# Kernel optimization log

Measured on AMD Instinct MI355X. Metric: run time of the kernel, lower is better.

Reference implementation:

```python
import jax, jax.numpy as jnp
import numpy as np

N_SIGMA = 2
FG_W = 1.0
W_INST, W_VAR, W_SEED = 1.0, 10.0, 1.0
N_IDS = 15  # instance ids 1..15 (0 = background)


def _xym(H, W, dtype):
    # torch buffer: xm varies along width, ym along height, linspace over 512 then sliced
    xm = jnp.broadcast_to(jnp.linspace(0.0, 1.0, 512)[:W][None, :], (H, W))
    ym = jnp.broadcast_to(jnp.linspace(0.0, 1.0, 512)[:H][:, None], (H, W))
    return jnp.stack([xm, ym], 0).astype(dtype)  # [2,H,W]


def _lovasz_hinge_flat(logits, gt):
    # canonical Lovasz hinge over a flat image; gt in {0,1} float
    signs = 2.0 * gt - 1.0
    errors = 1.0 - logits * signs
    order = jnp.argsort(-errors)
    errors_sorted = errors[order]
    gt_sorted = gt[order]
    gts = gt_sorted.sum()
    inter = gts - jnp.cumsum(gt_sorted)
    union = gts + jnp.cumsum(1.0 - gt_sorted)
    jacc = 1.0 - inter / union
    grad = jnp.concatenate([jacc[:1], jacc[1:] - jacc[:-1]])
    return jnp.dot(jax.nn.relu(errors_sorted), jax.lax.stop_gradient(grad))


def _loss(prediction, instances, labels):
    B, C, H, W = prediction.shape
    xym = _xym(H, W, prediction.dtype)
    spatial_emb = jnp.tanh(prediction[:, 0:2]) + xym           # [B,2,H,W]
    sigma = prediction[:, 2:2 + N_SIGMA]                       # [B,2,H,W]
    seed = jax.nn.sigmoid(prediction[:, 2 + N_SIGMA])          # [B,H,W]

    ids = jnp.arange(1, N_IDS + 1)
    maskf = (instances[:, None] == ids[None, :, None, None]).astype(prediction.dtype)  # [B,N,H,W]
    counts = maskf.sum((-2, -1))                               # [B,N]
    valid = counts > 0
    safe = jnp.maximum(counts, 1.0)

    centers = jnp.einsum('bchw,bnhw->bnc', spatial_emb, maskf) / safe[..., None]  # [B,N,2]
    s_mean = jnp.einsum('bchw,bnhw->bnc', sigma, maskf) / safe[..., None]         # [B,N,2]
    s_sg = jax.lax.stop_gradient(s_mean)

    # sum over mask of (sigma - s_sg)^2, expanded to avoid a [B,N,2,H,W] tensor
    e2 = jnp.einsum('bchw,bnhw->bnc', sigma * sigma, maskf)
    var_sum = e2 - 2.0 * s_sg * (s_mean * safe[..., None]) + s_sg * s_sg * counts[..., None]
    var_i = var_sum.sum(-1) / (N_SIGMA * safe)                 # torch.mean over [n_sigma, M]

    s_exp = jnp.exp(10.0 * s_mean)                             # [B,N,2] (grad flows, as in torch)
    dist_arg = jnp.zeros((B, N_IDS, H, W), prediction.dtype)
    for c in range(N_SIGMA):  # tiny fixed loop over 2 coordinate channels
        d = spatial_emb[:, c][:, None] - centers[:, :, c][..., None, None]
        dist_arg = dist_arg + s_exp[:, :, c][..., None, None] * d * d
    dist = jnp.exp(-dist_arg)                                  # [B,N,H,W]

    logits = (dist * 2.0 - 1.0).reshape(B * N_IDS, H * W)
    labs = maskf.reshape(B * N_IDS, H * W)
    inst_i = jax.vmap(_lovasz_hinge_flat)(logits, labs).reshape(B, N_IDS)

    seed_i = FG_W * jnp.einsum('bnhw,bnhw->bn', maskf,
                               (seed[:, None] - jax.lax.stop_gradient(dist)) ** 2)

    bg = (labels == 0).astype(prediction.dtype)
    seed_bg = jnp.einsum('bhw,bhw->b', bg, seed * seed)        # (seed - 0)^2 on background

    vf = valid.astype(prediction.dtype)
    obj = jnp.maximum(vf.sum(1), 1.0)
    inst_b = (vf * inst_i).sum(1) / obj
    var_b = (vf * var_i).sum(1) / obj
    seed_b = (seed_bg + (vf * seed_i).sum(1)) / (H * W)
    return jnp.mean(W_INST * inst_b + W_VAR * var_b + W_SEED * seed_b)


def setup_inputs() -> dict:
    key = jax.random.key(0)
    k1, k2, k3 = jax.random.split(key, 3)
    prediction = jax.random.normal(k1, (16, 5, 512, 512), dtype=jnp.float32)
    instances = jax.random.randint(k2, (16, 512, 512), 0, 16, dtype=jnp.int64)
    labels = jax.random.randint(k3, (16, 512, 512), 0, 2, dtype=jnp.int64)
    return {"prediction": prediction, "instances": instances, "labels": labels}


def reference(prediction, instances, labels):
    return _loss(prediction, instances, labels)
```

## Files before the change

### kernel.cpp

```cpp
#include <hip/hip_runtime.h>
#include <hip/hip_fp16.h>
#include <cmath>

#define BATCH 16
#define NID   15
#define NSEG  240
#define HW    262144
#define HEADB 65536
#define NSPL  8
#define NCHK  4
#define PREBLK 512
#define PSTRIDE 112

#define KFINEBASE 30208
#define KOVF 119
#define KTOT 2424

__device__ __forceinline__ int keyof(float d) {
  unsigned b = __float_as_uint(d);
  return (b >= 0x3B800000u) ? (int)((b >> 15) - KFINEBASE + KOVF) : (int)(b >> 23);
}
__device__ __forceinline__ void boundsof(int k, float* lo, float* hi) {
  if (k >= KOVF) {
    unsigned u = (unsigned)(k - KOVF + KFINEBASE) << 15;
    *lo = __uint_as_float(u);
    *hi = __uint_as_float(u + 32768u);
  } else {
    *lo = __uint_as_float((unsigned)k << 23);
    *hi = __uint_as_float((unsigned)(k + 1) << 23);
  }
}

__device__ __forceinline__ float fast_tanh(float x) {
  float e = __expf(2.0f * x);
  return 1.0f - 2.0f / (e + 1.0f);
}
__device__ __forceinline__ float fast_sigmoid(float x) {
  return 1.0f / (1.0f + __expf(-x));
}

struct Params { float cx, cy, e0, e1, var, valid, cnt; };
__device__ __forceinline__ Params calc_params(const float* __restrict__ st) {
  Params p;
  float cnt = st[0];
  float safe = fmaxf(cnt, 1.0f);
  p.cx = st[1] / safe;
  p.cy = st[2] / safe;
  float m0 = st[3] / safe, m1 = st[4] / safe;
  float v0 = st[5] - 2.0f * m0 * (m0 * safe) + m0 * m0 * cnt;
  float v1 = st[6] - 2.0f * m1 * (m1 * safe) + m1 * m1 * cnt;
  p.var = (v0 + v1) / (2.0f * safe);
  p.e0 = expf(10.0f * m0);
  p.e1 = expf(10.0f * m1);
  p.valid = (cnt > 0.f) ? 1.f : 0.f;
  p.cnt = cnt;
  return p;
}

__global__ void __launch_bounds__(256, 2)
pre_kernel(const float* __restrict__ pred, const int* __restrict__ inst,
           const int* __restrict__ lab, float* __restrict__ blockpart,
           unsigned* __restrict__ exyh, unsigned* __restrict__ tb8,
           unsigned* __restrict__ sd8) {
  __shared__ float ws[4][NID * 7 + 1];
  int tid = threadIdx.x;
  int w = tid >> 6, lane = tid & 63;
  int gid = blockIdx.x;
  int b = gid >> 5, c = gid & 31;
  const float* pb = pred + (size_t)b * 5 * HW;
  const int4* ip = (const int4*)(inst + (size_t)b * HW);
  const int4* lp = (const int4*)(lab + (size_t)b * HW);
  size_t bq = (size_t)b * (HW / 4);
  float acc[NID][7];
#pragma unroll
  for (int id = 0; id < NID; ++id)
#pragma unroll
    for (int s = 0; s < 7; ++s) acc[id][s] = 0.f;
  float bgacc = 0.f;
  for (int it = 0; it < 8; ++it) {
    int g = c * 2048 + it * 256 + tid;
    float4 v0 = ((const float4*)pb)[g];
    float4 v1 = ((const float4*)(pb + HW))[g];
    float4 v2 = ((const float4*)(pb + 2 * HW))[g];
    float4 v3 = ((const float4*)(pb + 3 * HW))[g];
    float4 v4 = ((const float4*)(pb + 4 * HW))[g];
    int4 t4 = ip[g];
    int4 l4 = lp[g];
    float p0a[4] = {v0.x, v0.y, v0.z, v0.w};
    float p1a[4] = {v1.x, v1.y, v1.z, v1.w};
    float p2a[4] = {v2.x, v2.y, v2.z, v2.w};
    float p3a[4] = {v3.x, v3.y, v3.z, v3.w};
    float p4a[4] = {v4.x, v4.y, v4.z, v4.w};
    int ta[4] = {t4.x, t4.y, t4.z, t4.w};
    int la[4] = {l4.x, l4.y, l4.z, l4.w};
    unsigned eo[4], tpack = 0, spack = 0;
    int px0 = g * 4;
#pragma unroll
    for (int k = 0; k < 4; ++k) {
      int px = px0 + k;
      float xm = (float)(px & 511) * (1.0f / 511.0f);
      float ym = (float)(px >> 9) * (1.0f / 511.0f);
      float ex = fast_tanh(p0a[k]) + xm;
      float ey = fast_tanh(p1a[k]) + ym;
      float sd = fast_sigmoid(p4a[k]);
      __half2 h = __floats2half2_rn(ex, ey);
      eo[k] = *reinterpret_cast<unsigned*>(&h);
      int t = ta[k];
      tpack |= ((unsigned)(t & 255)) << (8 * k);
      unsigned sq = (unsigned)(sd * 255.0f + 0.5f);
      spack |= (sq & 255u) << (8 * k);
      float p2 = p2a[k], p3 = p3a[k];
      float q2 = p2 * p2, q3 = p3 * p3;
#pragma unroll
      for (int id = 0; id < NID; ++id) {
        float pr = (t == id + 1) ? 1.0f : 0.0f;
        acc[id][0] += pr;
        acc[id][1] += pr * ex;
        acc[id][2] += pr * ey;
        acc[id][3] += pr * p2;
        acc[id][4] += pr * p3;
        acc[id][5] += pr * q2;
        acc[id][6] += pr * q3;
      }
      if (la[k] == 0) bgacc += sd * sd;
    }
    ((uint4*)exyh)[bq + g] = make_uint4(eo[0], eo[1], eo[2], eo[3]);
    tb8[bq + g] = tpack;
    sd8[bq + g] = spack;
  }
#pragma unroll
  for (int id = 0; id < NID; ++id)
#pragma unroll
    for (int s = 0; s < 7; ++s) {
      float v = acc[id][s];
      for (int off = 32; off > 0; off >>= 1) v += __shfl_down(v, off, 64);
      if (lane == 0) ws[w][id * 7 + s] = v;
    }
  for (int off = 32; off > 0; off >>= 1) bgacc += __shfl_down(bgacc, off, 64);
  if (lane == 0) ws[w][NID * 7] = bgacc;
  __syncthreads();
  float* bp = blockpart + (size_t)gid * PSTRIDE;
  for (int i = tid; i < NID * 7 + 1; i += 256)
    bp[i] = ws[0][i] + ws[1][i] + ws[2][i] + ws[3][i];
}

__global__ void reduce_kernel(const float* __restrict__ blockpart, float* __restrict__ stats,
                              float* __restrict__ seedbg) {
  int s = blockIdx.x;
  int b = blockIdx.y;
  int tid = threadIdx.x;
  float v = (tid < 32) ? blockpart[(size_t)(b * 32 + tid) * PSTRIDE + s] : 0.f;
  for (int off = 32; off > 0; off >>= 1) v += __shfl_down(v, off, 64);
  if (tid == 0) {
    if (s < NID * 7) {
      int id = s / 7, st = s % 7;
      stats[(b * NID + id) * 8 + st] = v;
    } else {
      seedbg[b] = v;
    }
  }
}

__global__ void __launch_bounds__(512)
hist_kernel(const unsigned* __restrict__ exyh, const unsigned* __restrict__ tb8,
            const unsigned* __restrict__ sd8, const float* __restrict__ stats,
            unsigned* __restrict__ partPN, float* __restrict__ seedi) {
  int split = blockIdx.x;
  int chunk = blockIdx.y;
  int b = blockIdx.z;
  int seg0 = chunk * 4;
  __shared__ unsigned lhist[4 * KTOT];
  __shared__ float prm[4][5];
  int tid = threadIdx.x;
  if (tid < 4) {
    int gs = seg0 + tid;
    if (gs < NID) {
      Params pp = calc_params(stats + (size_t)(b * NID + gs) * 8);
      prm[tid][0] = pp.cx; prm[tid][1] = pp.cy; prm[tid][2] = pp.e0; prm[tid][3] = pp.e1;
      prm[tid][4] = pp.valid;
    } else {
      prm[tid][4] = 0.f;
    }
  }
  for (int k = tid; k < 4 * KTOT; k += 512) lhist[k] = 0u;
  __syncthreads();
  float cxr[4], cyr[4], e0r[4], e1r[4];
  bool vr[4];
#pragma unroll
  for (int n = 0; n < 4; ++n) {
    cxr[n] = prm[n][0]; cyr[n] = prm[n][1]; e0r[n] = prm[n][2]; e1r[n] = prm[n][3];
    vr[n] = (prm[n][4] != 0.f);
  }
  const uint4* ev = (const uint4*)exyh + (size_t)b * (HW / 4);
  const unsigned* tv = tb8 + (size_t)b * (HW / 4);
  const unsigned* sv = sd8 + (size_t)b * (HW / 4);
  int lane = tid & 63;
  int wid = tid >> 6;
  int swl = (lane * 21) & 63;
  float sacc[4] = {0.f, 0.f, 0.f, 0.f};
  int g = split * 8192 + wid * 64 + swl;
  uint4 ee = ev[g];
  unsigned tp = tv[g];
  unsigned sp = sv[g];
  for (int it = 0; it < 16; ++it) {
    uint4 ne; unsigned ntp, nsp;
    int ng = g + 512;
    if (it < 15) { ne = ev[ng]; ntp = tv[ng]; nsp = sv[ng]; }
    unsigned ew[4] = {ee.x, ee.y, ee.z, ee.w};
#pragma unroll
    for (int k = 0; k < 4; ++k) {
      unsigned u = ew[k];
      __half2 h = *reinterpret_cast<__half2*>(&u);
      float2 e = __half22float2(h);
      int t = (int)((tp >> (8 * k)) & 255u);
#pragma unroll
      for (int n = 0; n < 4; ++n) {
        if (!vr[n]) continue;
        float dx = e.x - cxr[n];
        float dy = e.y - cyr[n];
        float d = __expf(-(e0r[n] * dx * dx + e1r[n] * dy * dy));
        int key = keyof(d);
        bool pos = (t == seg0 + n + 1);
        atomicAdd(&lhist[n * KTOT + key], pos ? 65536u : 1u);
        if (pos) {
          float sd = (float)((sp >> (8 * k)) & 255u) * (1.0f / 255.0f);
          float df = sd - d;
          sacc[n] += df * df;
        }
      }
    }
    if (it < 15) { ee = ne; tp = ntp; sp = nsp; g = ng; }
  }
#pragma unroll
  for (int n = 0; n < 4; ++n) {
    float v = sacc[n];
    for (int off = 32; off > 0; off >>= 1) v += __shfl_down(v, off, 64);
    if (lane == 0 && v != 0.f) atomicAdd(&seedi[b * NID + seg0 + n], v);
  }
  __syncthreads();
#pragma unroll
  for (int n = 0; n < 4; ++n) {
    int gs = seg0 + n;
    if (gs >= NID) break;
    size_t base = ((size_t)(b * NID + gs) * NSPL + split) * KTOT;
    for (int k = tid; k < KTOT; k += 512) partPN[base + k] = lhist[n * KTOT + k];
  }
}

__global__ void __launch_bounds__(1024)
lovasz_kernel(const unsigned* __restrict__ partPN, const float* __restrict__ stats,
              float* __restrict__ instAcc) {
  __shared__ int histP[KTOT];
  __shared__ int histN[KTOT];
  __shared__ int PreP[KTOT + 1];
  __shared__ int PreN[KTOT + 1];
  __shared__ int wtP[16];
  __shared__ int wtN[16];
  __shared__ float wred[16];
  __shared__ float prm[2];
  int seg = blockIdx.x;
  int tid = threadIdx.x;
  int lane = tid & 63, w = tid >> 6;
  if (tid == 0) {
    Params pp = calc_params(stats + (size_t)seg * 8);
    prm[0] = pp.valid;
    prm[1] = pp.cnt;
  }
  __syncthreads();
  if (prm[0] == 0.f) {
    if (tid == 0) instAcc[seg] = 0.f;
    return;
  }
  int P = (int)prm[1];
  int Nn = HW - P;
  for (int k = tid; k < KTOT; k += 1024) {
    int sp = 0, sn = 0;
#pragma unroll
    for (int s = 0; s < NSPL; ++s) {
      unsigned v = partPN[((size_t)seg * NSPL + s) * KTOT + k];
      sp += (int)(v >> 16);
      sn += (int)(v & 0xFFFFu);
    }
    histP[k] = sp;
    histN[k] = sn;
  }
  __syncthreads();
  {
    int base = tid * 3;
    int p0 = (base < KTOT) ? histP[base] : 0;
    int p1 = (base + 1 < KTOT) ? histP[base + 1] : 0;
    int p2 = (base + 2 < KTOT) ? histP[base + 2] : 0;
    int n0 = (base < KTOT) ? histN[base] : 0;
    int n1 = (base + 1 < KTOT) ? histN[base + 1] : 0;
    int n2 = (base + 2 < KTOT) ? histN[base + 2] : 0;
    int ap = p0 + p1 + p2, an = n0 + n1 + n2;
    int sip = ap, sin_ = an;
    for (int off = 1; off < 64; off <<= 1) {
      int up = __shfl_up(sip, off, 64);
      int un = __shfl_up(sin_, off, 64);
      if (lane >= off) { sip += up; sin_ += un; }
    }
    if (lane == 63) { wtP[w] = sip; wtN[w] = sin_; }
    __syncthreads();
    int woffP = 0, woffN = 0, totP = 0, totN = 0;
#pragma unroll
    for (int j = 0; j < 16; ++j) {
      int tp = wtP[j], tn = wtN[j];
      totP += tp; totN += tn;
      if (j < w) { woffP += tp; woffN += tn; }
    }
    int exP = woffP + sip - ap;
    int exN = woffN + sin_ - an;
    if (base < KTOT) {
      PreP[base] = exP;
      PreN[base] = exN;
    }
    if (base + 1 < KTOT) {
      PreP[base + 1] = exP + p0;
      PreN[base + 1] = exN + n0;
    }
    if (base + 2 < KTOT) {
      PreP[base + 2] = exP + p0 + p1;
      PreN[base + 2] = exN + n0 + n1;
    }
    if (tid == 0) {
      PreP[KTOT] = totP;
      PreN[KTOT] = totN;
    }
    __syncthreads();
  }
  float acc = 0.f;
  for (int k = tid; k < KTOT; k += 1024) {
    int hp = histP[k], hn = histN[k];
    if ((hp | hn) == 0) continue;
    float lo, hi;
    boundsof(k, &lo, &hi);
    float m = 0.5f * (lo + hi);
    m = fminf(m, __uint_as_float(0x3F7FFFFFu));
    float tv = 1.0f - m;
    int j = keyof(tv);
    float jlo, jhi;
    boundsof(j, &jlo, &jhi);
    float den = jhi - jlo;
    float fr = (den > 0.f) ? (tv - jlo) / den : 0.5f;
    fr = fminf(fmaxf(fr, 0.f), 1.f);
    if (hp) {
      float q = (float)(Nn - PreN[j + 1]) + (1.0f - fr) * (float)histN[j];
      float a = 2.0f - 2.0f * m;
      acc += (float)hp * a / ((float)P + q);
    }
    if (hn) {
      float p = (float)PreP[j] + fr * (float)histP[j];
      int R = Nn - PreN[k + 1];
      float u0 = 1.0f / (float)(P + R);
      float u1 = 1.0f / (float)(P + R + hn);
      acc += (2.0f * m) * ((float)P - p) * (u0 - u1);
    }
  }
  for (int off = 32; off > 0; off >>= 1) acc += __shfl_down(acc, off, 64);
  if (lane == 0) wred[w] = acc;
  __syncthreads();
  if (w == 0) {
    float v = (lane < 16) ? wred[lane] : 0.f;
    for (int off = 8; off > 0; off >>= 1) v += __shfl_down(v, off, 64);
    if (lane == 0) instAcc[seg] = v;
  }
}

__global__ void final_kernel(const float* __restrict__ stats, const float* __restrict__ instAcc,
                             const float* __restrict__ seediAcc, const float* __restrict__ seedbg,
                             float* __restrict__ out) {
  int b = threadIdx.x;
  __shared__ float red[64];
  float lb = 0.f;
  if (b < BATCH) {
    float sv = 0.f, si = 0.f, svar = 0.f, ssd = 0.f;
    for (int n = 0; n < NID; ++n) {
      Params pp = calc_params(stats + (size_t)(b * NID + n) * 8);
      float vf = pp.valid;
      sv += vf;
      si += vf * instAcc[b * NID + n];
      svar += vf * pp.var;
      ssd += vf * seediAcc[b * NID + n];
    }
    float obj = fmaxf(sv, 1.0f);
    lb = si / obj + 10.0f * (svar / obj) + (seedbg[b] + ssd) / (float)HW;
  }
  red[threadIdx.x] = lb;
  __syncthreads();
  for (int s = 32; s > 0; s >>= 1) {
    if (threadIdx.x < s) red[threadIdx.x] += red[threadIdx.x + s];
    __syncthreads();
  }
  if (threadIdx.x == 0) out[0] = red[0] / (float)BATCH;
}

extern "C" void kernel_launch(void* const* d_in, const int* in_sizes, int n_in,
                              void* d_out, int out_size, void* d_ws, size_t ws_size,
                              hipStream_t stream) {
  const float* pred = (const float*)d_in[0];
  const int* inst = (const int*)d_in[1];
  const int* lab = (const int*)d_in[2];
  float* out = (float*)d_out;

  float* wsf = (float*)d_ws;
  float* seediAcc = wsf;
  float* stats = wsf + 240;
  float* instAcc = wsf + 2160;
  float* seedbg = wsf + 2400;
  char* p = (char*)d_ws + HEADB;
  unsigned* exyh = (unsigned*)p;            p += (size_t)BATCH * HW * 4;
  unsigned* tb8 = (unsigned*)p;             p += (size_t)BATCH * HW;
  unsigned* sd8 = (unsigned*)p;             p += (size_t)BATCH * HW;
  unsigned* partPN = (unsigned*)p;          p += (size_t)NSEG * NSPL * KTOT * 4;
  float* blockpart = (float*)p;

  hipMemsetAsync(seediAcc, 0, 240 * sizeof(float), stream);
  pre_kernel<<<PREBLK, 256, 0, stream>>>(pred, inst, lab, blockpart, exyh, tb8, sd8);
  reduce_kernel<<<dim3(NID * 7 + 1, BATCH), 64, 0, stream>>>(blockpart, stats, seedbg);
  hist_kernel<<<dim3(NSPL, NCHK, BATCH), 512, 0, stream>>>(exyh, tb8, sd8, stats, partPN, seediAcc);
  lovasz_kernel<<<NSEG, 1024, 0, stream>>>(partPN, stats, instAcc);
  final_kernel<<<1, 64, 0, stream>>>(stats, instAcc, seediAcc, seedbg, out);
}
```

Baseline: 254.5 us.

## Vectorize per-id accumulators with packed float2 FMA and prefetch next tile

The per-instance moment accumulation in pre_kernel now uses 2-wide float vectors so the compiler can emit packed FMA instructions, roughly halving the accumulate instruction count. The loads for the next iteration are software-prefetched into registers, and the loop is left un-unrolled so memory latency can overlap compute. The launch_bounds occupancy hint is removed. The cost is more registers (padding lane plus prefetch buffers), which may lower occupancy.

After: 692.4 us. +172.0%, slower.

```diff
diff --git a/kernel.cpp b/kernel.cpp
--- a/kernel.cpp
+++ b/kernel.cpp
@@ -15,6 +15,8 @@
 #define KFINEBASE 30208
 #define KOVF 119
 #define KTOT 2424
+
+typedef float v2f __attribute__((ext_vector_type(2)));
 
 __device__ __forceinline__ int keyof(float d) {
   unsigned b = __float_as_uint(d);
@@ -57,11 +59,10 @@
   return p;
 }
 
-__global__ void __launch_bounds__(256, 2)
-pre_kernel(const float* __restrict__ pred, const int* __restrict__ inst,
-           const int* __restrict__ lab, float* __restrict__ blockpart,
-           unsigned* __restrict__ exyh, unsigned* __restrict__ tb8,
-           unsigned* __restrict__ sd8) {
+__global__ void pre_kernel(const float* __restrict__ pred, const int* __restrict__ inst,
+                           const int* __restrict__ lab, float* __restrict__ blockpart,
+                           unsigned* __restrict__ exyh, unsigned* __restrict__ tb8,
+                           unsigned* __restrict__ sd8) {
   __shared__ float ws[4][NID * 7 + 1];
   int tid = threadIdx.x;
   int w = tid >> 6, lane = tid & 63;
@@ -71,21 +72,35 @@
   const int4* ip = (const int4*)(inst + (size_t)b * HW);
   const int4* lp = (const int4*)(lab + (size_t)b * HW);
   size_t bq = (size_t)b * (HW / 4);
-  float acc[NID][7];
+  v2f acc[NID][4];
 #pragma unroll
   for (int id = 0; id < NID; ++id)
 #pragma unroll
-    for (int s = 0; s < 7; ++s) acc[id][s] = 0.f;
+    for (int s = 0; s < 4; ++s) acc[id][s] = (v2f)(0.f);
   float bgacc = 0.f;
+  int g0 = c * 2048 + tid;
+  float4 A0 = ((const float4*)pb)[g0];
+  float4 A1 = ((const float4*)(pb + HW))[g0];
+  float4 A2 = ((const float4*)(pb + 2 * HW))[g0];
+  float4 A3 = ((const float4*)(pb + 3 * HW))[g0];
+  float4 A4 = ((const float4*)(pb + 4 * HW))[g0];
+  int4 T4 = ip[g0];
+  int4 L4 = lp[g0];
+#pragma unroll 1
   for (int it = 0; it < 8; ++it) {
     int g = c * 2048 + it * 256 + tid;
-    float4 v0 = ((const float4*)pb)[g];
-    float4 v1 = ((const float4*)(pb + HW))[g];
-    float4 v2 = ((const float4*)(pb + 2 * HW))[g];
-    float4 v3 = ((const float4*)(pb + 3 * HW))[g];
-    float4 v4 = ((const float4*)(pb + 4 * HW))[g];
-    int4 t4 = ip[g];
-    int4 l4 = lp[g];
+    float4 v0 = A0, v1 = A1, v2 = A2, v3 = A3, v4 = A4;
+    int4 t4 = T4, l4 = L4;
+    if (it < 7) {
+      int gn = g + 256;
+      A0 = ((const float4*)pb)[gn];
+      A1 = ((const float4*)(pb + HW))[gn];
+      A2 = ((const float4*)(pb + 2 * HW))[gn];
+      A3 = ((const float4*)(pb + 3 * HW))[gn];
+      A4 = ((const float4*)(pb + 4 * HW))[gn];
+      T4 = ip[gn];
+      L4 = lp[gn];
+    }
     float p0a[4] = {v0.x, v0.y, v0.z, v0.w};
     float p1a[4] = {v1.x, v1.y, v1.z, v1.w};
     float p2a[4] = {v2.x, v2.y, v2.z, v2.w};
@@ -110,17 +125,18 @@
       unsigned sq = (unsigned)(sd * 255.0f + 0.5f);
       spack |= (sq & 255u) << (8 * k);
       float p2 = p2a[k], p3 = p3a[k];
-      float q2 = p2 * p2, q3 = p3 * p3;
+      v2f P01; P01.x = 1.0f; P01.y = ex;
+      v2f P23; P23.x = ey;   P23.y = p2;
+      v2f P45; P45.x = p3;   P45.y = p2 * p2;
+      v2f P67; P67.x = p3 * p3; P67.y = 0.f;
 #pragma unroll
       for (int id = 0; id < NID; ++id) {
         float pr = (t == id + 1) ? 1.0f : 0.0f;
-        acc[id][0] += pr;
-        acc[id][1] += pr * ex;
-        acc[id][2] += pr * ey;
-        acc[id][3] += pr * p2;
-        acc[id][4] += pr * p3;
-        acc[id][5] += pr * q2;
-        acc[id][6] += pr * q3;
+        v2f prv; prv.x = pr; prv.y = pr;
+        acc[id][0] = prv * P01 + acc[id][0];
+        acc[id][1] = prv * P23 + acc[id][1];
+        acc[id][2] = prv * P45 + acc[id][2];
+        acc[id][3] = prv * P67 + acc[id][3];
       }
       if (la[k] == 0) bgacc += sd * sd;
     }
@@ -129,13 +145,16 @@
     sd8[bq + g] = spack;
   }
 #pragma unroll
-  for (int id = 0; id < NID; ++id)
+  for (int id = 0; id < NID; ++id) {
+    float vals7[7] = {acc[id][0].x, acc[id][0].y, acc[id][1].x, acc[id][1].y,
+                      acc[id][2].x, acc[id][2].y, acc[id][3].x};
 #pragma unroll
     for (int s = 0; s < 7; ++s) {
-      float v = acc[id][s];
+      float v = vals7[s];
       for (int off = 32; off > 0; off >>= 1) v += __shfl_down(v, off, 64);
       if (lane == 0) ws[w][id * 7 + s] = v;
     }
+  }
   for (int off = 32; off > 0; off >>= 1) bgacc += __shfl_down(bgacc, off, 64);
   if (lane == 0) ws[w][NID * 7] = bgacc;
   __syncthreads();
```
